# Kernel optimization log

Measured on AMD Instinct MI355X. Metric: run time of the kernel, lower is better.

## Reference

```python
import jax, jax.numpy as jnp
import numpy as np

N_LAYERS = 2
H_DIR = 200           # hidden_dim // 2 per direction
IN_SIZE = 400         # == hidden_dim
WORD_VOCAB, WORD_DIM = 100000, 300
POS_VOCAB, POS_DIM = 50, 100
SEQ = 512


def _lstm_dir(x, Wih, Whh, bih, bhh, reverse):
    # x: [n, in]; Wih: [4H, in]; Whh: [4H, H]; bih/bhh: [4H]
    H = Whh.shape[1]
    pre = x @ Wih.T + (bih + bhh)  # [n, 4H], hoist input projection out of scan

    def step(carry, p):
        h, c = carry
        g = p + h @ Whh.T
        i, f, gg, o = jnp.split(g, 4, axis=-1)  # torch gate order i,f,g,o
        i, f, o = jax.nn.sigmoid(i), jax.nn.sigmoid(f), jax.nn.sigmoid(o)
        c = f * c + i * jnp.tanh(gg)
        h = o * jnp.tanh(c)
        return (h, c), h

    init = (jnp.zeros((H,), x.dtype), jnp.zeros((H,), x.dtype))
    _, hs = jax.lax.scan(step, init, pre, reverse=reverse)
    return hs  # [n, H], aligned with input order


def setup_inputs() -> dict:
    key = jax.random.key(0)
    ks = jax.random.split(key, 20)
    s = 0.05
    inp = {}
    inp['word_emb'] = jax.random.normal(ks[0], (WORD_VOCAB, WORD_DIM), jnp.float32) * s
    inp['pos_emb'] = jax.random.normal(ks[1], (POS_VOCAB, POS_DIM), jnp.float32) * s
    # stacked LSTM params: [layer, direction, ...]; both layers have 400-dim input
    inp['Wih'] = jax.random.normal(ks[2], (N_LAYERS, 2, 4 * H_DIR, IN_SIZE), jnp.float32) * s
    inp['Whh'] = jax.random.normal(ks[3], (N_LAYERS, 2, 4 * H_DIR, H_DIR), jnp.float32) * s
    inp['bih'] = jax.random.normal(ks[4], (N_LAYERS, 2, 4 * H_DIR), jnp.float32) * s
    inp['bhh'] = jax.random.normal(ks[5], (N_LAYERS, 2, 4 * H_DIR), jnp.float32) * s
    inp['W_h1'] = jax.random.normal(ks[6], (IN_SIZE, IN_SIZE), jnp.float32) * s
    inp['b_h1'] = jax.random.normal(ks[7], (IN_SIZE,), jnp.float32) * s
    inp['W_h2'] = jax.random.normal(ks[8], (IN_SIZE, IN_SIZE), jnp.float32) * s
    inp['b_h2'] = jax.random.normal(ks[9], (IN_SIZE,), jnp.float32) * s
    inp['W_d1'] = jax.random.normal(ks[10], (IN_SIZE, IN_SIZE), jnp.float32) * s
    inp['b_d1'] = jax.random.normal(ks[11], (IN_SIZE,), jnp.float32) * s
    inp['W_d2'] = jax.random.normal(ks[12], (IN_SIZE, IN_SIZE), jnp.float32) * s
    inp['b_d2'] = jax.random.normal(ks[13], (IN_SIZE,), jnp.float32) * s
    inp['W_bi'] = jax.random.normal(ks[14], (IN_SIZE, IN_SIZE), jnp.float32) * s  # Bilinear weight [1,in,in] squeezed
    inp['b_bi'] = jax.random.normal(ks[15], (1,), jnp.float32) * s
    inp['sentence_word_indices'] = jax.random.randint(ks[16], (SEQ,), 0, WORD_VOCAB, jnp.int32)
    inp['sentence_pos_indices'] = jax.random.randint(ks[17], (SEQ,), 0, POS_VOCAB, jnp.int32)
    return inp


def reference(word_emb, pos_emb, Wih, Whh, bih, bhh,
              W_h1, b_h1, W_h2, b_h2, W_d1, b_d1, W_d2, b_d2,
              W_bi, b_bi, sentence_word_indices, sentence_pos_indices):
    # embedding lookup + concat -> [n, 400]
    x = jnp.concatenate([word_emb[sentence_word_indices],
                         pos_emb[sentence_pos_indices]], axis=1)
    # 2-layer bidirectional LSTM (batch=1, zero initial state)
    for l in range(N_LAYERS):
        fwd = _lstm_dir(x, Wih[l, 0], Whh[l, 0], bih[l, 0], bhh[l, 0], reverse=False)
        bwd = _lstm_dir(x, Wih[l, 1], Whh[l, 1], bih[l, 1], bhh[l, 1], reverse=True)
        x = jnp.concatenate([fwd, bwd], axis=-1)  # [n, 400]
    # batched head/dependent MLPs (original recomputes these per (i,j) pair)
    head = jax.nn.relu(jax.nn.relu(x @ W_h1.T + b_h1) @ W_h2.T + b_h2)  # [n, 400]
    dep = jax.nn.relu(jax.nn.relu(x @ W_d1.T + b_d1) @ W_d2.T + b_d2)   # [n, 400]
    # bilinear score matrix: score[i,j] = head_i^T W dep_j + b
    matrix = jnp.einsum('id,de,je->ij', head, W_bi, dep) + b_bi[0]  # [n, n]
    return matrix
```

## Files before the change

kernel.cpp:

```cpp
#include <hip/hip_runtime.h>
#include <hip/hip_bf16.h>
#include <cstdint>
#include <cstddef>


#define TSEQ 512
#define HDIR 200
#define INSZ 400
#define G4   800

typedef unsigned long long u64;

__global__ void k_embed(const float* __restrict__ we, const float* __restrict__ pe,
                        const int* __restrict__ wi, const int* __restrict__ pi,
                        float* __restrict__ x) {
  int t = blockIdx.x;
  int w = wi[t], p = pi[t];
  const float* wrow = we + (size_t)w * 300;
  const float* prow = pe + (size_t)p * 100;
  for (int j = threadIdx.x; j < INSZ; j += blockDim.x)
    x[(size_t)t * INSZ + j] = (j < 300) ? wrow[j] : prow[j - 300];
}

__global__ void k_add(const float* __restrict__ a, const float* __restrict__ b,
                      float* __restrict__ o, int n) {
  int i = blockIdx.x * blockDim.x + threadIdx.x;
  if (i < n) o[i] = a[i] + b[i];
}

__device__ __forceinline__ void gemm_bt_body(
    const float* __restrict__ A, const float* __restrict__ B,
    const float* __restrict__ bias, float* __restrict__ C,
    int m, int k, int bias_mode, int do_relu, int bx, int by)
{
  __shared__ float As[16][68];
  __shared__ float Bs[16][68];
  const int tid = threadIdx.x;
  const int tx = tid & 15, ty = tid >> 4;
  const int row0 = by << 6, col0 = bx << 6;
  const int lr = tid >> 2;
  const int kq = (tid & 3) << 2;
  float acc[4][4] = {};

  for (int ks = 0; ks < k; ks += 16) {
    float4 a4 = *(const float4*)(A + (size_t)(row0 + lr) * k + ks + kq);
    float4 b4 = make_float4(0.f, 0.f, 0.f, 0.f);
    if (col0 + lr < m)
      b4 = *(const float4*)(B + (size_t)(col0 + lr) * k + ks + kq);
    As[kq + 0][lr] = a4.x; As[kq + 1][lr] = a4.y; As[kq + 2][lr] = a4.z; As[kq + 3][lr] = a4.w;
    Bs[kq + 0][lr] = b4.x; Bs[kq + 1][lr] = b4.y; Bs[kq + 2][lr] = b4.z; Bs[kq + 3][lr] = b4.w;
    __syncthreads();
#pragma unroll
    for (int kk = 0; kk < 16; ++kk) {
      const float4 av = *(const float4*)&As[kk][ty << 2];
      const float4 bv = *(const float4*)&Bs[kk][tx << 2];
      const float a_[4] = {av.x, av.y, av.z, av.w};
      const float b_[4] = {bv.x, bv.y, bv.z, bv.w};
#pragma unroll
      for (int i = 0; i < 4; ++i)
#pragma unroll
        for (int j = 0; j < 4; ++j)
          acc[i][j] += a_[i] * b_[j];
    }
    __syncthreads();
  }

#pragma unroll
  for (int i = 0; i < 4; ++i) {
    const int r = row0 + (ty << 2) + i;
#pragma unroll
    for (int j = 0; j < 4; ++j) {
      const int c = col0 + (tx << 2) + j;
      if (c < m) {
        float v = acc[i][j];
        if (bias_mode == 1) v += bias[c];
        else if (bias_mode == 2) v += bias[0];
        if (do_relu) v = fmaxf(v, 0.f);
        C[(size_t)r * m + c] = v;
      }
    }
  }
}

__global__ __launch_bounds__(256) void k_gemm_bt(
    const float* __restrict__ A, const float* __restrict__ B,
    const float* __restrict__ bias, float* __restrict__ C,
    int m, int k, int bias_mode, int do_relu)
{
  gemm_bt_body(A, B, bias, C, m, k, bias_mode, do_relu, blockIdx.x, blockIdx.y);
}

__global__ __launch_bounds__(256) void k_gemm_bt_dual(
    const float* __restrict__ A0, const float* __restrict__ B0,
    const float* __restrict__ bias0, float* __restrict__ C0,
    const float* __restrict__ A1, const float* __restrict__ B1,
    const float* __restrict__ bias1, float* __restrict__ C1,
    int m, int k, int bias_mode, int do_relu)
{
  const float* A = blockIdx.z ? A1 : A0;
  const float* B = blockIdx.z ? B1 : B0;
  const float* bias = blockIdx.z ? bias1 : bias0;
  float* C = blockIdx.z ? C1 : C0;
  gemm_bt_body(A, B, bias, C, m, k, bias_mode, do_relu, blockIdx.x, blockIdx.y);
}

__global__ __launch_bounds__(448, 1) void k_scan(
    const float* __restrict__ Whh,
    const float* __restrict__ pre,
    float* __restrict__ hs,
    u64* hbuf,
    int layer)
{
  const int bid = blockIdx.x;
  if ((bid & 7) > 1) return;
  const int dir = bid & 7;
  const int p = bid >> 3;
  const int tid = threadIdx.x;
  const int rr = tid >> 1;
  const int u = tid & 1;
  const bool act = rr < HDIR;
  const int g = rr / 50;
  const int q = rr - g * 50;
  const int grow = act ? (g * HDIR + p * 50 + q) : 0;
  const int own0 = p * 50;

  __shared__ float h_lds[HDIR];
  __shared__ float g_lds[HDIR];

  float4 w[25];
  {
    const float* wrow = Whh + ((size_t)(layer * 2 + dir) * G4 + grow) * HDIR + u * 100;
#pragma unroll
    for (int i = 0; i < 25; ++i) w[i] = *(const float4*)(wrow + i * 4);
  }

  for (int i = tid; i < HDIR; i += 448) h_lds[i] = 0.f;
  float c_state = 0.f;
  u64* hb_dir = hbuf + dir * HDIR;
  __syncthreads();

  for (int t = 0; t < TSEQ; ++t) {
    const int inrow = dir ? (TSEQ - 1 - t) : t;

    float preval = 0.f;
    if (act && u == 0)
      preval = pre[(size_t)inrow * 1600 + dir * G4 + grow];

    if (t > 0 && tid < 150) {
      const int j = (tid < own0) ? tid : tid + 50;
      const u64* src = hb_dir + (size_t)(t & 1) * 400 + j;
      u64 v;
      do {
        v = __hip_atomic_load(src, __ATOMIC_RELAXED, __HIP_MEMORY_SCOPE_AGENT);
      } while ((unsigned)(v >> 32) < (unsigned)t);
      union { unsigned uu; float f; } cv; cv.uu = (unsigned)v;
      h_lds[j] = cv.f;
    }
    __syncthreads();

    if (act) {
      float4 acc = make_float4(0.f, 0.f, 0.f, 0.f);
      const float* hb = h_lds + u * 100;
#pragma unroll
      for (int i = 0; i < 25; ++i) {
        const float4 hv = *(const float4*)(hb + i * 4);
        acc.x += w[i].x * hv.x; acc.y += w[i].y * hv.y;
        acc.z += w[i].z * hv.z; acc.w += w[i].w * hv.w;
      }
      float tot = acc.x + acc.y + acc.z + acc.w;
      tot += __shfl_xor(tot, 1);
      if (u == 0) {
        const float gv = tot + preval;
        const float xx = (g == 2) ? 2.f * gv : gv;
        const float s = 1.f / (1.f + __expf(-xx));
        g_lds[rr] = (g == 2) ? (2.f * s - 1.f) : s;
      }
    }
    __syncthreads();

    if (tid < 50) {
      const float ai = g_lds[tid];
      const float af = g_lds[50 + tid];
      const float ag = g_lds[100 + tid];
      const float ao = g_lds[150 + tid];
      c_state = af * c_state + ai * ag;
      const float th = 2.f / (1.f + __expf(-2.f * c_state)) - 1.f;
      const float hv = ao * th;
      if (t != TSEQ - 1) {
        union { float f; unsigned uu; } cv; cv.f = hv;
        const u64 pk = ((u64)(unsigned)(t + 1) << 32) | cv.uu;
        __hip_atomic_store(hb_dir + (size_t)((t + 1) & 1) * 400 + own0 + tid,
                           pk, __ATOMIC_RELAXED, __HIP_MEMORY_SCOPE_AGENT);
      }
      h_lds[own0 + tid] = hv;
      hs[(size_t)inrow * INSZ + dir * HDIR + own0 + tid] = hv;
    }
  }
}

extern "C" void kernel_launch(void* const* d_in, const int* in_sizes, int n_in,
                              void* d_out, int out_size, void* d_ws, size_t ws_size,
                              hipStream_t stream)
{
  const float* we   = (const float*)d_in[0];
  const float* pe   = (const float*)d_in[1];
  const float* Wih  = (const float*)d_in[2];
  const float* Whh  = (const float*)d_in[3];
  const float* bih  = (const float*)d_in[4];
  const float* bhh  = (const float*)d_in[5];
  const float* W_h1 = (const float*)d_in[6];
  const float* b_h1 = (const float*)d_in[7];
  const float* W_h2 = (const float*)d_in[8];
  const float* b_h2 = (const float*)d_in[9];
  const float* W_d1 = (const float*)d_in[10];
  const float* b_d1 = (const float*)d_in[11];
  const float* W_d2 = (const float*)d_in[12];
  const float* b_d2 = (const float*)d_in[13];
  const float* W_bi = (const float*)d_in[14];
  const float* b_bi = (const float*)d_in[15];
  const int*   wi   = (const int*)d_in[16];
  const int*   pi   = (const int*)d_in[17];
  float* out = (float*)d_out;

  float* ws = (float*)d_ws;
  float* x0   = ws;
  float* pre  = ws + 204800;
  float* h1   = ws + 1024000;
  float* h2   = ws + 1228800;
  float* m1h  = ws + 1433600;
  float* m1d  = ws + 1638400;
  float* m2   = ws + 1843200;
  float* m3   = ws + 2048000;
  float* t1   = ws + 2252800;
  float* bsum = ws + 2457600;
  u64* hbuf0  = (u64*)(ws + 2461696);
  u64* hbuf1  = hbuf0 + 800;

  hipMemsetAsync(hbuf0, 0, 2 * 800 * sizeof(u64), stream);
  k_embed<<<TSEQ, 128, 0, stream>>>(we, pe, wi, pi, x0);
  k_add<<<(3200 + 255) / 256, 256, 0, stream>>>(bih, bhh, bsum, 3200);

  k_gemm_bt<<<dim3(25, 8), 256, 0, stream>>>(x0, Wih, bsum, pre, 1600, 400, 1, 0);
  k_scan<<<26, 448, 0, stream>>>(Whh, pre, h1, hbuf0, 0);
  k_gemm_bt<<<dim3(25, 8), 256, 0, stream>>>(h1, Wih + 1600 * 400, bsum + 1600, pre, 1600, 400, 1, 0);
  k_scan<<<26, 448, 0, stream>>>(Whh, pre, h2, hbuf1, 1);

  k_gemm_bt_dual<<<dim3(7, 8, 2), 256, 0, stream>>>(h2, W_h1, b_h1, m1h,
                                                    h2, W_d1, b_d1, m1d, 400, 400, 1, 1);
  k_gemm_bt_dual<<<dim3(7, 8, 2), 256, 0, stream>>>(m1h, W_h2, b_h2, m2,
                                                    m1d, W_d2, b_d2, m3, 400, 400, 1, 1);

  k_gemm_bt<<<dim3(7, 8), 256, 0, stream>>>(m3, W_bi, nullptr, t1, 400, 400, 0, 0);
  k_gemm_bt<<<dim3(8, 8), 256, 0, stream>>>(m2, t1, b_bi, out, 512, 400, 2, 0);
}
```

Before: 1.612 ms.

## Split LSTM recurrence across 26 single-wave blocks with shuffle-based gate exchange

Result: slower. 2.623 ms (+62.8%).

```diff
diff --git a/kernel.cpp b/kernel.cpp
--- a/kernel.cpp
+++ b/kernel.cpp
@@ -104,95 +104,91 @@
   gemm_bt_body(A, B, bias, C, m, k, bias_mode, do_relu, blockIdx.x, blockIdx.y);
 }
 
-__global__ __launch_bounds__(448, 1) void k_scan(
-    const float* __restrict__ Whh,
-    const float* __restrict__ pre,
-    float* __restrict__ hs,
-    u64* hbuf,
-    int layer)
+__global__ __launch_bounds__(64) __attribute__((amdgpu_waves_per_eu(1, 1)))
+void k_scan(const float* __restrict__ Whh,
+            const float* __restrict__ pre,
+            float* __restrict__ hs,
+            u64* hbuf,
+            int layer)
 {
   const int bid = blockIdx.x;
-  if ((bid & 7) > 1) return;
-  const int dir = bid & 7;
-  const int p = bid >> 3;
+  const int dir = bid & 1;
+  const int pb = bid >> 1;
+  const int own0 = pb * 16;
+  const int own_n = (own0 + 16 <= HDIR) ? 16 : (HDIR - own0);
   const int tid = threadIdx.x;
-  const int rr = tid >> 1;
-  const int u = tid & 1;
-  const bool act = rr < HDIR;
-  const int g = rr / 50;
-  const int q = rr - g * 50;
-  const int grow = act ? (g * HDIR + p * 50 + q) : 0;
-  const int own0 = p * 50;
+  const int gate = tid >> 4;
+  const int hloc = tid & 15;
+  const bool act = hloc < own_n;
+  const int grow = gate * HDIR + own0 + (act ? hloc : 0);
 
   __shared__ float h_lds[HDIR];
-  __shared__ float g_lds[HDIR];
-
-  float4 w[25];
+
+  float4 w[50];
   {
-    const float* wrow = Whh + ((size_t)(layer * 2 + dir) * G4 + grow) * HDIR + u * 100;
-#pragma unroll
-    for (int i = 0; i < 25; ++i) w[i] = *(const float4*)(wrow + i * 4);
-  }
-
-  for (int i = tid; i < HDIR; i += 448) h_lds[i] = 0.f;
+    const float* wrow = Whh + ((size_t)(layer * 2 + dir) * G4 + grow) * HDIR;
+#pragma unroll
+    for (int i = 0; i < 50; ++i) w[i] = *(const float4*)(wrow + i * 4);
+  }
+
+  for (int i = tid; i < HDIR; i += 64) h_lds[i] = 0.f;
   float c_state = 0.f;
-  u64* hb_dir = hbuf + dir * HDIR;
   __syncthreads();
 
   for (int t = 0; t < TSEQ; ++t) {
     const int inrow = dir ? (TSEQ - 1 - t) : t;
-
-    float preval = 0.f;
-    if (act && u == 0)
-      preval = pre[(size_t)inrow * 1600 + dir * G4 + grow];
-
-    if (t > 0 && tid < 150) {
-      const int j = (tid < own0) ? tid : tid + 50;
-      const u64* src = hb_dir + (size_t)(t & 1) * 400 + j;
-      u64 v;
-      do {
-        v = __hip_atomic_load(src, __ATOMIC_RELAXED, __HIP_MEMORY_SCOPE_AGENT);
-      } while ((unsigned)(v >> 32) < (unsigned)t);
-      union { unsigned uu; float f; } cv; cv.uu = (unsigned)v;
-      h_lds[j] = cv.f;
+    const float preval = act ? pre[(size_t)inrow * 1600 + dir * G4 + grow] : 0.f;
+
+    if (t > 0) {
+      const u64* base = hbuf + (size_t)(t & 1) * 400 + dir * HDIR;
+      u64 va = __hip_atomic_load(base + tid,       __ATOMIC_RELAXED, __HIP_MEMORY_SCOPE_AGENT);
+      u64 vb = __hip_atomic_load(base + tid + 64,  __ATOMIC_RELAXED, __HIP_MEMORY_SCOPE_AGENT);
+      u64 vc = __hip_atomic_load(base + tid + 128, __ATOMIC_RELAXED, __HIP_MEMORY_SCOPE_AGENT);
+      u64 vd = (tid < 8) ? __hip_atomic_load(base + tid + 192, __ATOMIC_RELAXED, __HIP_MEMORY_SCOPE_AGENT)
+                         : ((u64)0xFFFFFFFFu << 32);
+      while ((unsigned)(va >> 32) < (unsigned)t)
+        va = __hip_atomic_load(base + tid,       __ATOMIC_RELAXED, __HIP_MEMORY_SCOPE_AGENT);
+      while ((unsigned)(vb >> 32) < (unsigned)t)
+        vb = __hip_atomic_load(base + tid + 64,  __ATOMIC_RELAXED, __HIP_MEMORY_SCOPE_AGENT);
+      while ((unsigned)(vc >> 32) < (unsigned)t)
+        vc = __hip_atomic_load(base + tid + 128, __ATOMIC_RELAXED, __HIP_MEMORY_SCOPE_AGENT);
+      while ((unsigned)(vd >> 32) < (unsigned)t)
+        vd = __hip_atomic_load(base + tid + 192, __ATOMIC_RELAXED, __HIP_MEMORY_SCOPE_AGENT);
+      union { unsigned uu; float f; } c0, c1, c2, c3;
+      c0.uu = (unsigned)va; c1.uu = (unsigned)vb; c2.uu = (unsigned)vc; c3.uu = (unsigned)vd;
+      h_lds[tid] = c0.f; h_lds[tid + 64] = c1.f; h_lds[tid + 128] = c2.f;
+      if (tid < 8) h_lds[tid + 192] = c3.f;
     }
     __syncthreads();
 
-    if (act) {
-      float4 acc = make_float4(0.f, 0.f, 0.f, 0.f);
-      const float* hb = h_lds + u * 100;
-#pragma unroll
-      for (int i = 0; i < 25; ++i) {
-        const float4 hv = *(const float4*)(hb + i * 4);
-        acc.x += w[i].x * hv.x; acc.y += w[i].y * hv.y;
-        acc.z += w[i].z * hv.z; acc.w += w[i].w * hv.w;
-      }
-      float tot = acc.x + acc.y + acc.z + acc.w;
-      tot += __shfl_xor(tot, 1);
-      if (u == 0) {
-        const float gv = tot + preval;
-        const float xx = (g == 2) ? 2.f * gv : gv;
-        const float s = 1.f / (1.f + __expf(-xx));
-        g_lds[rr] = (g == 2) ? (2.f * s - 1.f) : s;
-      }
-    }
-    __syncthreads();
-
-    if (tid < 50) {
-      const float ai = g_lds[tid];
-      const float af = g_lds[50 + tid];
-      const float ag = g_lds[100 + tid];
-      const float ao = g_lds[150 + tid];
+    float4 a4 = make_float4(0.f, 0.f, 0.f, 0.f);
+#pragma unroll
+    for (int i = 0; i < 50; ++i) {
+      const float4 hv = *(const float4*)(h_lds + i * 4);
+      a4.x += w[i].x * hv.x; a4.y += w[i].y * hv.y;
+      a4.z += w[i].z * hv.z; a4.w += w[i].w * hv.w;
+    }
+    const float gv = a4.x + a4.y + a4.z + a4.w + preval;
+
+    const float xx = (gate == 2) ? 2.f * gv : gv;
+    const float s = 1.f / (1.f + __expf(-xx));
+    const float av = (gate == 2) ? (2.f * s - 1.f) : s;
+
+    const float ai = __shfl(av, hloc);
+    const float af = __shfl(av, hloc + 16);
+    const float ag = __shfl(av, hloc + 32);
+    const float ao = __shfl(av, hloc + 48);
+
+    if (tid < own_n) {
       c_state = af * c_state + ai * ag;
       const float th = 2.f / (1.f + __expf(-2.f * c_state)) - 1.f;
       const float hv = ao * th;
       if (t != TSEQ - 1) {
         union { float f; unsigned uu; } cv; cv.f = hv;
         const u64 pk = ((u64)(unsigned)(t + 1) << 32) | cv.uu;
-        __hip_atomic_store(hb_dir + (size_t)((t + 1) & 1) * 400 + own0 + tid,
+        __hip_atomic_store(hbuf + (size_t)((t + 1) & 1) * 400 + dir * HDIR + own0 + tid,
                            pk, __ATOMIC_RELAXED, __HIP_MEMORY_SCOPE_AGENT);
       }
-      h_lds[own0 + tid] = hv;
       hs[(size_t)inrow * INSZ + dir * HDIR + own0 + tid] = hv;
     }
   }
@@ -241,9 +237,9 @@
   k_add<<<(3200 + 255) / 256, 256, 0, stream>>>(bih, bhh, bsum, 3200);
 
   k_gemm_bt<<<dim3(25, 8), 256, 0, stream>>>(x0, Wih, bsum, pre, 1600, 400, 1, 0);
-  k_scan<<<26, 448, 0, stream>>>(Whh, pre, h1, hbuf0, 0);
+  k_scan<<<26, 64, 0, stream>>>(Whh, pre, h1, hbuf0, 0);
   k_gemm_bt<<<dim3(25, 8), 256, 0, stream>>>(h1, Wih + 1600 * 400, bsum + 1600, pre, 1600, 400, 1, 0);
-  k_scan<<<26, 448, 0, stream>>>(Whh, pre, h2, hbuf1, 1);
+  k_scan<<<26, 64, 0, stream>>>(Whh, pre, h2, hbuf1, 1);
 
   k_gemm_bt_dual<<<dim3(7, 8, 2), 256, 0, stream>>>(h2, W_h1, b_h1, m1h,
                                                     h2, W_d1, b_d1, m1d, 400, 400, 1, 1);
```

## Split LSTM recurrence across 20 blocks per direction and reload weights each step

Applied to the files above, without the earlier changes.

Result: slower. 2.380 ms (+47.6%).

```diff
diff --git a/kernel.cpp b/kernel.cpp
--- a/kernel.cpp
+++ b/kernel.cpp
@@ -8,6 +8,9 @@
 #define HDIR 200
 #define INSZ 400
 #define G4   800
+#define NPART 20
+#define HPB  10
+#define ROWS 40
 
 typedef unsigned long long u64;
 
@@ -104,50 +107,54 @@
   gemm_bt_body(A, B, bias, C, m, k, bias_mode, do_relu, blockIdx.x, blockIdx.y);
 }
 
-__global__ __launch_bounds__(448, 1) void k_scan(
-    const float* __restrict__ Whh,
-    const float* __restrict__ pre,
-    float* __restrict__ hs,
-    u64* hbuf,
-    int layer)
+__global__ __launch_bounds__(192, 2)
+void k_scan(const float* __restrict__ Whh,
+            const float* __restrict__ pre,
+            float* __restrict__ hs,
+            u64* hbuf,
+            int layer)
 {
   const int bid = blockIdx.x;
-  if ((bid & 7) > 1) return;
-  const int dir = bid & 7;
-  const int p = bid >> 3;
+  const int dir = bid & 1;
+  const int p = bid >> 1;
   const int tid = threadIdx.x;
-  const int rr = tid >> 1;
-  const int u = tid & 1;
-  const bool act = rr < HDIR;
-  const int g = rr / 50;
-  const int q = rr - g * 50;
-  const int grow = act ? (g * HDIR + p * 50 + q) : 0;
-  const int own0 = p * 50;
+  const int rr = tid >> 2;
+  const int u = tid & 3;
+  const bool act = rr < ROWS;
+  const int g = rr / HPB;
+  const int q = rr - g * HPB;
+  const int grow = act ? (g * HDIR + p * HPB + q) : 0;
+  const int own0 = p * HPB;
 
   __shared__ float h_lds[HDIR];
-  __shared__ float g_lds[HDIR];
-
-  float4 w[25];
-  {
-    const float* wrow = Whh + ((size_t)(layer * 2 + dir) * G4 + grow) * HDIR + u * 100;
-#pragma unroll
-    for (int i = 0; i < 25; ++i) w[i] = *(const float4*)(wrow + i * 4);
-  }
-
-  for (int i = tid; i < HDIR; i += 448) h_lds[i] = 0.f;
+  __shared__ float g_lds[ROWS];
+
+  const float* wbase = Whh + ((size_t)(layer * 2 + dir) * G4 + grow) * HDIR + u * 50;
+  u64* hb_dir = hbuf + dir * HDIR;
+
+  for (int i = tid; i < HDIR; i += 192) h_lds[i] = 0.f;
   float c_state = 0.f;
-  u64* hb_dir = hbuf + dir * HDIR;
+  int ofs = 0;
   __syncthreads();
 
   for (int t = 0; t < TSEQ; ++t) {
     const int inrow = dir ? (TSEQ - 1 - t) : t;
 
+    float2 wv[25];
     float preval = 0.f;
-    if (act && u == 0)
-      preval = pre[(size_t)inrow * 1600 + dir * G4 + grow];
-
-    if (t > 0 && tid < 150) {
-      const int j = (tid < own0) ? tid : tid + 50;
+    if (act) {
+      int c = ofs;
+#pragma unroll
+      for (int i = 0; i < 25; ++i) {
+        wv[i] = *(const float2*)(wbase + c * 2);
+        c = (c == 24) ? 0 : c + 1;
+      }
+      if (u == 0) preval = pre[(size_t)inrow * 1600 + dir * G4 + grow];
+    }
+    __builtin_amdgcn_sched_barrier(0);
+
+    if (t > 0 && tid < HDIR - HPB) {
+      const int j = (tid < own0) ? tid : tid + HPB;
       const u64* src = hb_dir + (size_t)(t & 1) * 400 + j;
       u64 v;
       do {
@@ -159,16 +166,18 @@
     __syncthreads();
 
     if (act) {
-      float4 acc = make_float4(0.f, 0.f, 0.f, 0.f);
-      const float* hb = h_lds + u * 100;
+      float ax = 0.f, ay = 0.f;
+      const float* hb = h_lds + u * 50;
+      int c = ofs;
 #pragma unroll
       for (int i = 0; i < 25; ++i) {
-        const float4 hv = *(const float4*)(hb + i * 4);
-        acc.x += w[i].x * hv.x; acc.y += w[i].y * hv.y;
-        acc.z += w[i].z * hv.z; acc.w += w[i].w * hv.w;
-      }
-      float tot = acc.x + acc.y + acc.z + acc.w;
+        const float2 hv = *(const float2*)(hb + c * 2);
+        ax += wv[i].x * hv.x; ay += wv[i].y * hv.y;
+        c = (c == 24) ? 0 : c + 1;
+      }
+      float tot = ax + ay;
       tot += __shfl_xor(tot, 1);
+      tot += __shfl_xor(tot, 2);
       if (u == 0) {
         const float gv = tot + preval;
         const float xx = (g == 2) ? 2.f * gv : gv;
@@ -178,11 +187,11 @@
     }
     __syncthreads();
 
-    if (tid < 50) {
+    if (tid < HPB) {
       const float ai = g_lds[tid];
-      const float af = g_lds[50 + tid];
-      const float ag = g_lds[100 + tid];
-      const float ao = g_lds[150 + tid];
+      const float af = g_lds[HPB + tid];
+      const float ag = g_lds[2 * HPB + tid];
+      const float ao = g_lds[3 * HPB + tid];
       c_state = af * c_state + ai * ag;
       const float th = 2.f / (1.f + __expf(-2.f * c_state)) - 1.f;
       const float hv = ao * th;
@@ -195,6 +204,7 @@
       h_lds[own0 + tid] = hv;
       hs[(size_t)inrow * INSZ + dir * HDIR + own0 + tid] = hv;
     }
+    ofs = (ofs == 24) ? 0 : ofs + 1;
   }
 }
 
@@ -241,9 +251,9 @@
   k_add<<<(3200 + 255) / 256, 256, 0, stream>>>(bih, bhh, bsum, 3200);
 
   k_gemm_bt<<<dim3(25, 8), 256, 0, stream>>>(x0, Wih, bsum, pre, 1600, 400, 1, 0);
-  k_scan<<<26, 448, 0, stream>>>(Whh, pre, h1, hbuf0, 0);
+  k_scan<<<40, 192, 0, stream>>>(Whh, pre, h1, hbuf0, 0);
   k_gemm_bt<<<dim3(25, 8), 256, 0, stream>>>(h1, Wih + 1600 * 400, bsum + 1600, pre, 1600, 400, 1, 0);
-  k_scan<<<26, 448, 0, stream>>>(Whh, pre, h2, hbuf1, 1);
+  k_scan<<<40, 192, 0, stream>>>(Whh, pre, h2, hbuf1, 1);
 
   k_gemm_bt_dual<<<dim3(7, 8, 2), 256, 0, stream>>>(h2, W_h1, b_h1, m1h,
                                                     h2, W_d1, b_d1, m1d, 400, 400, 1, 1);
```

## Split LSTM scan across 8 blocks per direction with LDS-resident weights

Applied to the files above, without the earlier changes.

Measured after the change: 1.811 ms. 12.4% more time.

```diff
diff --git a/kernel.cpp b/kernel.cpp
--- a/kernel.cpp
+++ b/kernel.cpp
@@ -8,6 +8,8 @@
 #define HDIR 200
 #define INSZ 400
 #define G4   800
+#define HPB  25
+#define SW   204
 
 typedef unsigned long long u64;
 
@@ -104,39 +106,41 @@
   gemm_bt_body(A, B, bias, C, m, k, bias_mode, do_relu, blockIdx.x, blockIdx.y);
 }
 
-__global__ __launch_bounds__(448, 1) void k_scan(
-    const float* __restrict__ Whh,
-    const float* __restrict__ pre,
-    float* __restrict__ hs,
-    u64* hbuf,
-    int layer)
+__global__ __launch_bounds__(256)
+void k_scan(const float* __restrict__ Whh,
+            const float* __restrict__ pre,
+            float* __restrict__ hs,
+            u64* hbuf,
+            int layer)
 {
   const int bid = blockIdx.x;
   if ((bid & 7) > 1) return;
   const int dir = bid & 7;
   const int p = bid >> 3;
   const int tid = threadIdx.x;
-  const int rr = tid >> 1;
+  const int hq = tid >> 3;
+  const int g = (tid >> 1) & 3;
   const int u = tid & 1;
-  const bool act = rr < HDIR;
-  const int g = rr / 50;
-  const int q = rr - g * 50;
-  const int grow = act ? (g * HDIR + p * 50 + q) : 0;
-  const int own0 = p * 50;
-
-  __shared__ float h_lds[HDIR];
-  __shared__ float g_lds[HDIR];
-
-  float4 w[25];
-  {
-    const float* wrow = Whh + ((size_t)(layer * 2 + dir) * G4 + grow) * HDIR + u * 100;
-#pragma unroll
-    for (int i = 0; i < 25; ++i) w[i] = *(const float4*)(wrow + i * 4);
-  }
-
-  for (int i = tid; i < HDIR; i += 448) h_lds[i] = 0.f;
+  const bool act = tid < 200;
+  const int own0 = p * HPB;
+  const int grow = g * HDIR + own0 + hq;
+
+  extern __shared__ float smem[];
+  float* w_lds = smem;
+  float* h_lds = smem + 100 * SW;
+
+  const float* WhhL = Whh + (size_t)(layer * 2 + dir) * G4 * HDIR;
+  u64* hb_dir = hbuf + dir * HDIR;
+
+  for (int idx = tid; idx < 100 * 50; idx += 256) {
+    const int lr = idx / 50;
+    const int c4 = idx - lr * 50;
+    const int gg = lr / 25, qq = lr - gg * 25;
+    const float4 v = *(const float4*)(WhhL + ((size_t)(gg * HDIR + own0 + qq)) * HDIR + c4 * 4);
+    *(float4*)(w_lds + lr * SW + c4 * 4) = v;
+  }
+  for (int i = tid; i < 400; i += 256) h_lds[i] = 0.f;
   float c_state = 0.f;
-  u64* hb_dir = hbuf + dir * HDIR;
   __syncthreads();
 
   for (int t = 0; t < TSEQ; ++t) {
@@ -146,54 +150,54 @@
     if (act && u == 0)
       preval = pre[(size_t)inrow * 1600 + dir * G4 + grow];
 
-    if (t > 0 && tid < 150) {
-      const int j = (tid < own0) ? tid : tid + 50;
+    if (t > 0 && tid < HDIR - HPB) {
+      const int j = (tid < own0) ? tid : tid + HPB;
       const u64* src = hb_dir + (size_t)(t & 1) * 400 + j;
       u64 v;
       do {
         v = __hip_atomic_load(src, __ATOMIC_RELAXED, __HIP_MEMORY_SCOPE_AGENT);
       } while ((unsigned)(v >> 32) < (unsigned)t);
       union { unsigned uu; float f; } cv; cv.uu = (unsigned)v;
-      h_lds[j] = cv.f;
+      h_lds[(t & 1) * HDIR + j] = cv.f;
     }
     __syncthreads();
 
+    float av = 0.f;
     if (act) {
-      float4 acc = make_float4(0.f, 0.f, 0.f, 0.f);
-      const float* hb = h_lds + u * 100;
+      const float* hb = h_lds + (t & 1) * HDIR + u * 100;
+      const float* wb = w_lds + (g * 25 + hq) * SW + u * 100;
+      float ax = 0.f, ay = 0.f, az = 0.f, aw = 0.f;
 #pragma unroll
       for (int i = 0; i < 25; ++i) {
+        const float4 wv = *(const float4*)(wb + i * 4);
         const float4 hv = *(const float4*)(hb + i * 4);
-        acc.x += w[i].x * hv.x; acc.y += w[i].y * hv.y;
-        acc.z += w[i].z * hv.z; acc.w += w[i].w * hv.w;
+        ax += wv.x * hv.x; ay += wv.y * hv.y;
+        az += wv.z * hv.z; aw += wv.w * hv.w;
       }
-      float tot = acc.x + acc.y + acc.z + acc.w;
+      float tot = ax + ay + az + aw;
       tot += __shfl_xor(tot, 1);
-      if (u == 0) {
-        const float gv = tot + preval;
-        const float xx = (g == 2) ? 2.f * gv : gv;
-        const float s = 1.f / (1.f + __expf(-xx));
-        g_lds[rr] = (g == 2) ? (2.f * s - 1.f) : s;
-      }
-    }
-    __syncthreads();
-
-    if (tid < 50) {
-      const float ai = g_lds[tid];
-      const float af = g_lds[50 + tid];
-      const float ag = g_lds[100 + tid];
-      const float ao = g_lds[150 + tid];
-      c_state = af * c_state + ai * ag;
+      const float gv = tot + preval;
+      const float xx = (g == 2) ? 2.f * gv : gv;
+      const float s = 1.f / (1.f + __expf(-xx));
+      av = (g == 2) ? (2.f * s - 1.f) : s;
+    }
+    const int lb = (tid & 63) & ~7;
+    const float af = __shfl(av, lb + 2);
+    const float ag = __shfl(av, lb + 4);
+    const float ao = __shfl(av, lb + 6);
+
+    if (act && (tid & 7) == 0) {
+      c_state = af * c_state + av * ag;
       const float th = 2.f / (1.f + __expf(-2.f * c_state)) - 1.f;
       const float hv = ao * th;
       if (t != TSEQ - 1) {
         union { float f; unsigned uu; } cv; cv.f = hv;
         const u64 pk = ((u64)(unsigned)(t + 1) << 32) | cv.uu;
-        __hip_atomic_store(hb_dir + (size_t)((t + 1) & 1) * 400 + own0 + tid,
+        __hip_atomic_store(hb_dir + (size_t)((t + 1) & 1) * 400 + own0 + hq,
                            pk, __ATOMIC_RELAXED, __HIP_MEMORY_SCOPE_AGENT);
       }
-      h_lds[own0 + tid] = hv;
-      hs[(size_t)inrow * INSZ + dir * HDIR + own0 + tid] = hv;
+      h_lds[((t + 1) & 1) * HDIR + own0 + hq] = hv;
+      hs[(size_t)inrow * INSZ + dir * HDIR + own0 + hq] = hv;
     }
   }
 }
@@ -236,14 +240,20 @@
   u64* hbuf0  = (u64*)(ws + 2461696);
   u64* hbuf1  = hbuf0 + 800;
 
+  const int SMEM = (100 * SW + 400) * 4;
+  static int attr_done = 0;
+  hipFuncSetAttribute((const void*)k_scan,
+                      hipFuncAttributeMaxDynamicSharedMemorySize, SMEM);
+  (void)attr_done;
+
   hipMemsetAsync(hbuf0, 0, 2 * 800 * sizeof(u64), stream);
   k_embed<<<TSEQ, 128, 0, stream>>>(we, pe, wi, pi, x0);
   k_add<<<(3200 + 255) / 256, 256, 0, stream>>>(bih, bhh, bsum, 3200);
 
   k_gemm_bt<<<dim3(25, 8), 256, 0, stream>>>(x0, Wih, bsum, pre, 1600, 400, 1, 0);
-  k_scan<<<26, 448, 0, stream>>>(Whh, pre, h1, hbuf0, 0);
+  k_scan<<<64, 256, SMEM, stream>>>(Whh, pre, h1, hbuf0, 0);
   k_gemm_bt<<<dim3(25, 8), 256, 0, stream>>>(h1, Wih + 1600 * 400, bsum + 1600, pre, 1600, 400, 1, 0);
-  k_scan<<<26, 448, 0, stream>>>(Whh, pre, h2, hbuf1, 1);
+  k_scan<<<64, 256, SMEM, stream>>>(Whh, pre, h2, hbuf1, 1);
 
   k_gemm_bt_dual<<<dim3(7, 8, 2), 256, 0, stream>>>(h2, W_h1, b_h1, m1h,
                                                     h2, W_d1, b_d1, m1d, 400, 400, 1, 1);
```
